# Kernel optimization log

Hardware: AMD Instinct MI355X
Metric: run time of the kernel (lower is better)

## Reference

```python
import jax, jax.numpy as jnp
import numpy as np

N_SRC = 100000
N_DST = 100000
E = 500000
D = 128
L = 2


def _sage(x_src, x_dst, e_src, e_dst, W_self, W_neigh, b):
    # DGL SAGEConv('mean'): out = x_dst @ W_self^T + mean_neighbors(x_src) @ W_neigh^T + b
    n_dst = x_dst.shape[0]
    msg_sum = jax.ops.segment_sum(x_src[e_src], e_dst, num_segments=n_dst)  # [n_dst, D]
    deg = jax.ops.segment_sum(jnp.ones((e_dst.shape[0],), x_src.dtype), e_dst, num_segments=n_dst)
    h_neigh = msg_sum / jnp.maximum(deg, 1.0)[:, None]  # isolated nodes -> 0
    return x_dst @ W_self.T + h_neigh @ W_neigh.T + b


def setup_inputs() -> dict:
    key = jax.random.key(0)
    ks = jax.random.split(key, 10)
    s = 1.0 / np.sqrt(D)
    return {
        "x_src": jax.random.normal(ks[0], (N_SRC, D), jnp.float32),
        "x_dst": jax.random.normal(ks[1], (N_DST, D), jnp.float32),
        "e_src": jax.random.randint(ks[2], (E,), 0, N_SRC, jnp.int32),
        "e_dst": jax.random.randint(ks[3], (E,), 0, N_DST, jnp.int32),
        "W_ship_self": jax.random.normal(ks[4], (L, D, D), jnp.float32) * s,
        "W_ship_neigh": jax.random.normal(ks[5], (L, D, D), jnp.float32) * s,
        "b_ship": jnp.zeros((L, D), jnp.float32),
        "W_rev_self": jax.random.normal(ks[6], (L, D, D), jnp.float32) * s,
        "W_rev_neigh": jax.random.normal(ks[7], (L, D, D), jnp.float32) * s,
        "b_rev": jnp.zeros((L, D), jnp.float32),
    }


def reference(x_src, x_dst, e_src, e_dst, W_ship_self, W_ship_neigh, b_ship,
              W_rev_self, W_rev_neigh, b_rev):
    h_s, h_d = x_src, x_dst
    n_layers = W_ship_self.shape[0]
    for l in range(n_layers):
        # ('source','ship','destination'): messages source -> destination
        new_d = _sage(h_s, h_d, e_src, e_dst, W_ship_self[l], W_ship_neigh[l], b_ship[l])
        # ('destination','rev_ship','source'): messages destination -> source
        new_s = _sage(h_d, h_s, e_dst, e_src, W_rev_self[l], W_rev_neigh[l], b_rev[l])
        h_d = jax.nn.relu(new_d)
        h_s = jax.nn.relu(new_s)
        # dropout p=0.0 (eval) -> identity
    return h_s, h_d
```

## Files before the change

kernel.cpp:

```cpp
#include <hip/hip_runtime.h>
#include <hip/hip_bf16.h>

#define NN 100000
#define EDGES 500000
#define DD 128
#define NBKT 196
#define SLACK 3584
#define CHUNK 4096
#define BPD ((EDGES + CHUNK - 1) / CHUNK)


typedef short bf16x8 __attribute__((ext_vector_type(8)));
typedef float f32x4  __attribute__((ext_vector_type(4)));
typedef float f32x2  __attribute__((ext_vector_type(2)));

__device__ __forceinline__ unsigned short f2bf(float f) {
    unsigned u = __float_as_uint(f);
    u += 0x7fffu + ((u >> 16) & 1u);
    return (unsigned short)(u >> 16);
}

__global__ void f2bx_kernel(const float* __restrict__ a, const float* __restrict__ b,
                            unsigned short* __restrict__ oaR, unsigned short* __restrict__ oaB,
                            unsigned short* __restrict__ obR, unsigned short* __restrict__ obB) {
    const float* in = blockIdx.y ? b : a;
    unsigned short* outR = blockIdx.y ? obR : oaR;
    unsigned short* outB = blockIdx.y ? obB : oaB;
    int t = blockIdx.x * 256 + threadIdx.x;
    int row = t >> 4, sl = t & 15;
    const float4* src = (const float4*)in + row * 32 + sl * 2;
    float4 v0 = src[0], v1 = src[1];
    uint4 o;
    o.x = (unsigned)f2bf(v0.x) | ((unsigned)f2bf(v0.y) << 16);
    o.y = (unsigned)f2bf(v0.z) | ((unsigned)f2bf(v0.w) << 16);
    o.z = (unsigned)f2bf(v1.x) | ((unsigned)f2bf(v1.y) << 16);
    o.w = (unsigned)f2bf(v1.z) | ((unsigned)f2bf(v1.w) << 16);
    *(uint4*)(outR + row * 128 + sl * 8) = o;
    int boff = (row >> 4) * 2048 + (sl >> 2) * 512 + (sl & 3) * 128 + (row & 15) * 8;
    *(uint4*)(outB + boff) = o;
}

__global__ void f2bw_kernel(const float* __restrict__ w0, const float* __restrict__ w1,
                            const float* __restrict__ w2, const float* __restrict__ w3,
                            unsigned short* __restrict__ o0, unsigned short* __restrict__ o1,
                            unsigned short* __restrict__ o2, unsigned short* __restrict__ o3) {
    const float* in; unsigned short* out;
    switch (blockIdx.y) {
        case 0: in = w0; out = o0; break;
        case 1: in = w1; out = o1; break;
        case 2: in = w2; out = o2; break;
        default: in = w3; out = o3; break;
    }
    int i = blockIdx.x * 256 + threadIdx.x;
    float4 v = ((const float4*)in)[i];
    ushort4 o;
    o.x = f2bf(v.x); o.y = f2bf(v.y); o.z = f2bf(v.z); o.w = f2bf(v.w);
    ((ushort4*)out)[i] = o;
}

__global__ __launch_bounds__(256) void bin_scatter_kernel(
    const int* __restrict__ e_src, const int* __restrict__ e_dst,
    int* __restrict__ gcnt,
    unsigned* __restrict__ recbin)
{
    const int dir = blockIdx.y;
    const int t = threadIdx.x;
    const int c0 = blockIdx.x * CHUNK;
    const int nvalid = min(CHUNK, EDGES - c0);
    const int* __restrict__ TGT = dir ? e_src : e_dst;
    const int* __restrict__ PAY = dir ? e_dst : e_src;

    __shared__ int hist[256];
    __shared__ int lbase[256];
    __shared__ int lofs[256];
    __shared__ int scanA[256], scanB[256];
    __shared__ int laddr[CHUNK];
    __shared__ unsigned lrec[CHUNK];

    hist[t] = 0;
    __syncthreads();

    int myb[16], myslot[16];
    unsigned myrec[16];
    #pragma unroll
    for (int j = 0; j < 16; ++j) {
        int e = c0 + j * 256 + t;
        myb[j] = -1;
        if (e < EDGES) {
            int tgt = TGT[e], pay = PAY[e];
            int b = tgt >> 9;
            myb[j] = b;
            myrec[j] = ((unsigned)pay << 9) | (unsigned)(tgt & 511);
            myslot[j] = atomicAdd(&hist[b], 1);
        }
    }
    __syncthreads();
    int cnt = hist[t];
    lbase[t] = (cnt > 0) ? atomicAdd(&gcnt[dir * 256 + t], cnt) : 0;
    scanA[t] = cnt;
    __syncthreads();
    int* pa = scanA; int* pb = scanB;
    for (int d = 1; d < 256; d <<= 1) {
        pb[t] = pa[t] + (t >= d ? pa[t - d] : 0);
        __syncthreads();
        int* tmp = pa; pa = pb; pb = tmp;
    }
    lofs[t] = pa[t] - cnt;
    __syncthreads();
    #pragma unroll
    for (int j = 0; j < 16; ++j) {
        if (myb[j] >= 0) {
            int b = myb[j];
            int pos = lofs[b] + myslot[j];
            int g = lbase[b] + myslot[j];
            lrec[pos] = myrec[j];
            laddr[pos] = (g < SLACK) ? (b * SLACK + g) : -1;
        }
    }
    __syncthreads();
    unsigned* __restrict__ out = recbin + (size_t)dir * NBKT * SLACK;
    #pragma unroll
    for (int j = 0; j < 16; ++j) {
        int i = j * 256 + t;
        if (i < nvalid) {
            int a = laddr[i];
            if (a >= 0) out[a] = lrec[i];
        }
    }
}

__global__ void bucket_scan_kernel(const int* __restrict__ gcnt, int* __restrict__ csr_base) {
    int t = threadIdx.x;
    __shared__ int A[256], B[256];
    for (int dir = 0; dir < 2; ++dir) {
        int c = (t < NBKT) ? min(gcnt[dir * 256 + t], SLACK) : 0;
        A[t] = c;
        __syncthreads();
        int* pa = A; int* pb = B;
        for (int d = 1; d < 256; d <<= 1) {
            pb[t] = pa[t] + (t >= d ? pa[t - d] : 0);
            __syncthreads();
            int* tmp = pa; pa = pb; pb = tmp;
        }
        if (t < NBKT) csr_base[dir * 200 + t] = pa[t] - c;
        if (t == 0)   csr_base[dir * 200 + NBKT] = pa[255];
        __syncthreads();
    }
}

__global__ __launch_bounds__(256) void fine_place_kernel(
    const unsigned* __restrict__ recbin, const int* __restrict__ gcnt,
    const int* __restrict__ csr_base,
    int* __restrict__ rp_dst, int* __restrict__ rp_src,
    float* __restrict__ inv_dst, float* __restrict__ inv_src,
    int* __restrict__ csr_dst, int* __restrict__ csr_src)
{
    const int dir = blockIdx.y;
    const int bkt = blockIdx.x;
    const int t = threadIdx.x;
    int*   __restrict__ rp  = dir ? rp_src  : rp_dst;
    float* __restrict__ inv = dir ? inv_src : inv_dst;
    int*   __restrict__ csr = dir ? csr_src : csr_dst;
    const unsigned* __restrict__ recs = recbin + ((size_t)dir * NBKT + bkt) * SLACK;
    const int cnt = min(gcnt[dir * 256 + bkt], SLACK);
    const int cbase = csr_base[dir * 200 + bkt];
    const int n0 = bkt * 512;

    __shared__ int deg[512];
    __shared__ int sA[512], sB[512];
    __shared__ int cur[512];
    deg[t] = 0; deg[t + 256] = 0;
    __syncthreads();
    for (int i = t; i < cnt; i += 256)
        atomicAdd(&deg[recs[i] & 511u], 1);
    __syncthreads();
    sA[t] = deg[t]; sA[t + 256] = deg[t + 256];
    __syncthreads();
    int* pa = sA; int* pb = sB;
    for (int d = 1; d < 512; d <<= 1) {
        pb[t]       = pa[t]       + (t >= d           ? pa[t - d]       : 0);
        pb[t + 256] = pa[t + 256] + ((t + 256) >= d   ? pa[t + 256 - d] : 0);
        __syncthreads();
        int* tmp = pa; pa = pb; pb = tmp;
    }
    #pragma unroll
    for (int k = 0; k < 2; ++k) {
        int i = t + k * 256;
        int off = pa[i] - deg[i];
        cur[i] = off;
        int node = n0 + i;
        if (node < NN) {
            rp[node] = cbase + off;
            inv[node] = 1.0f / (float)max(deg[i], 1);
        }
    }
    if (bkt == NBKT - 1 && t == 0) rp[NN] = csr_base[dir * 200 + NBKT];
    __syncthreads();
    for (int i = t; i < cnt; i += 256) {
        unsigned r = recs[i];
        int p = atomicAdd(&cur[r & 511u], 1);
        csr[cbase + p] = (int)(r >> 9);
    }
}

__global__ __launch_bounds__(256) void aggregate5_kernel(
    const unsigned short* __restrict__ h0, const int* __restrict__ rp0,
    const int* __restrict__ csr0, unsigned short* __restrict__ ag0,
    const unsigned short* __restrict__ h1, const int* __restrict__ rp1,
    const int* __restrict__ csr1, unsigned short* __restrict__ ag1)
{
    const int dir = blockIdx.y;
    const unsigned short* __restrict__ h = dir ? h1 : h0;
    const int* __restrict__ rp   = dir ? rp1 : rp0;
    const int* __restrict__ csr  = dir ? csr1 : csr0;
    unsigned short* __restrict__ agg = dir ? ag1 : ag0;

    const int t  = blockIdx.x * 256 + threadIdx.x;
    const int g  = t >> 4;
    const int sl = t & 15;

    const int beg = rp[g], end = rp[g + 1];
    const unsigned short* __restrict__ hp = h + sl * 8;

    f32x2 acc[4];
    #pragma unroll
    for (int k = 0; k < 4; ++k) acc[k] = (f32x2){0.f, 0.f};

    int cidx[8];
    #pragma unroll
    for (int j = 0; j < 8; ++j)
        cidx[j] = (beg + j < end) ? csr[beg + j] : -1;

    bf16x8 v[8];
    #pragma unroll
    for (int j = 0; j < 8; ++j)
        if (cidx[j] >= 0)
            v[j] = *(const bf16x8*)(hp + (size_t)cidx[j] * DD);

    #pragma unroll
    for (int j = 0; j < 8; ++j) {
        if (cidx[j] >= 0) {
            const unsigned* pu = (const unsigned*)&v[j];
            #pragma unroll
            for (int k = 0; k < 4; ++k) {
                unsigned u = pu[k];
                acc[k] += (f32x2){__uint_as_float(u << 16),
                                  __uint_as_float(u & 0xffff0000u)};
            }
        }
    }

    for (int i = beg + 8; i < end; ++i) {
        int c = csr[i];
        bf16x8 wv = *(const bf16x8*)(hp + (size_t)c * DD);
        const unsigned* pu = (const unsigned*)&wv;
        #pragma unroll
        for (int k = 0; k < 4; ++k) {
            unsigned u = pu[k];
            acc[k] += (f32x2){__uint_as_float(u << 16),
                              __uint_as_float(u & 0xffff0000u)};
        }
    }

    const float sc = 1.0f / (float)max(end - beg, 1);
    uint4 ov;
    ov.x = (unsigned)f2bf(acc[0].x * sc) | ((unsigned)f2bf(acc[0].y * sc) << 16);
    ov.y = (unsigned)f2bf(acc[1].x * sc) | ((unsigned)f2bf(acc[1].y * sc) << 16);
    ov.z = (unsigned)f2bf(acc[2].x * sc) | ((unsigned)f2bf(acc[2].y * sc) << 16);
    ov.w = (unsigned)f2bf(acc[3].x * sc) | ((unsigned)f2bf(acc[3].y * sc) << 16);
    int boff = (g >> 4) * 2048 + (sl >> 2) * 512 + (sl & 3) * 128 + (g & 15) * 8;
    *(uint4*)(agg + boff) = ov;
}

__global__ __launch_bounds__(512, 4) void mfma_gemm9_kernel(
    const unsigned short* __restrict__ Hs0, const unsigned short* __restrict__ Ha0,
    const unsigned short* __restrict__ Ws0, const unsigned short* __restrict__ Wn0,
    const float* __restrict__ bias0, float* __restrict__ outF0,
    unsigned short* __restrict__ outR0, unsigned short* __restrict__ outB0,
    const unsigned short* __restrict__ Hs1, const unsigned short* __restrict__ Ha1,
    const unsigned short* __restrict__ Ws1, const unsigned short* __restrict__ Wn1,
    const float* __restrict__ bias1, float* __restrict__ outF1,
    unsigned short* __restrict__ outR1, unsigned short* __restrict__ outB1,
    int M)
{
    const int dir = blockIdx.y;
    const unsigned short* __restrict__ Hself = dir ? Hs1 : Hs0;
    const unsigned short* __restrict__ Hagg  = dir ? Ha1 : Ha0;
    const unsigned short* __restrict__ Wself = dir ? Ws1 : Ws0;
    const unsigned short* __restrict__ Wneigh= dir ? Wn1 : Wn0;
    const float* __restrict__ bias = dir ? bias1 : bias0;
    float* __restrict__ outF = dir ? outF1 : outF0;
    unsigned short* __restrict__ outR = dir ? outR1 : outR0;
    unsigned short* __restrict__ outB = dir ? outB1 : outB0;

    __shared__ __align__(16) unsigned short sW[128 * 256];
    const int tid  = threadIdx.x;
    const int lane = tid & 63;
    const int w    = tid >> 6;
    const int row0 = blockIdx.x * 256;

    #pragma unroll
    for (int i = 0; i < 8; ++i) {
        int q = i * 512 + tid;
        int n = q >> 5, c = q & 31;
        const unsigned short* src = (c < 16) ? (Wself + n * 128 + c * 8)
                                             : (Wneigh + n * 128 + (c - 16) * 8);
        int d = n * 256 + (c & 24) * 8 + (((c ^ n) & 7) * 8);
        *(uint4*)(sW + d) = *(const uint4*)src;
    }

    const int mbase = (w >> 1) * 64;
    const int nbase = (w & 1) * 64;
    const int l15 = lane & 15;
    const int l4  = lane >> 4;
    const int MT  = M >> 4;

    int aoff[4];
    #pragma unroll
    for (int mt = 0; mt < 4; ++mt) {
        int rt = ((row0 + mbase) >> 4) + mt;
        if (rt >= MT) rt = MT - 1;
        aoff[mt] = rt * 2048 + lane * 8;
    }

    f32x4 acc[4][4];
    #pragma unroll
    for (int mt = 0; mt < 4; ++mt)
        #pragma unroll
        for (int nt = 0; nt < 4; ++nt) acc[mt][nt] = (f32x4){0.f, 0.f, 0.f, 0.f};

    __syncthreads();

    bf16x8 a_cur[4], a_nxt[4];
    #pragma unroll
    for (int mt = 0; mt < 4; ++mt) a_cur[mt] = *(const bf16x8*)(Hself + aoff[mt]);

    #pragma unroll
    for (int ks = 0; ks < 8; ++ks) {
        if (ks < 7) {
            const int ks1 = ks + 1;
            const int col = (ks1 & 3) * 512;
            const unsigned short* __restrict__ base = (ks1 < 4) ? Hself : Hagg;
            #pragma unroll
            for (int mt = 0; mt < 4; ++mt)
                a_nxt[mt] = *(const bf16x8*)(base + aoff[mt] + col);
        }
        const int c = ks * 4 + l4;
        bf16x8 b[4];
        #pragma unroll
        for (int nt = 0; nt < 4; ++nt) {
            int n = nbase + nt * 16 + l15;
            b[nt] = *(const bf16x8*)(sW + n * 256 + (c & 24) * 8 + (((c ^ n) & 7) * 8));
        }
        #pragma unroll
        for (int mt = 0; mt < 4; ++mt) {
            acc[mt][0] = __builtin_amdgcn_mfma_f32_16x16x32_bf16(a_cur[mt], b[0], acc[mt][0], 0, 0, 0);
            acc[mt][1] = __builtin_amdgcn_mfma_f32_16x16x32_bf16(a_cur[mt], b[1], acc[mt][1], 0, 0, 0);
            acc[mt][2] = __builtin_amdgcn_mfma_f32_16x16x32_bf16(a_cur[mt], b[2], acc[mt][2], 0, 0, 0);
            acc[mt][3] = __builtin_amdgcn_mfma_f32_16x16x32_bf16(a_cur[mt], b[3], acc[mt][3], 0, 0, 0);
        }
        #pragma unroll
        for (int mt = 0; mt < 4; ++mt) a_cur[mt] = a_nxt[mt];
    }

    #pragma unroll
    for (int nt = 0; nt < 4; ++nt) {
        int col = nbase + nt * 16 + l15;
        float bj = bias[col];
        #pragma unroll
        for (int mt = 0; mt < 4; ++mt) {
            #pragma unroll
            for (int r = 0; r < 4; ++r) {
                int grow = row0 + mbase + mt * 16 + l4 * 4 + r;
                if (grow < M) {
                    float v = fmaxf(acc[mt][nt][r] + bj, 0.f);
                    if (outF) {
                        outF[(size_t)grow * 128 + col] = v;
                    } else {
                        unsigned short bv = f2bf(v);
                        outR[(size_t)grow * 128 + col] = bv;
                        int bo = (grow >> 4) * 2048 + (col >> 5) * 512
                               + ((col >> 3) & 3) * 128 + (grow & 15) * 8 + (col & 7);
                        outB[bo] = bv;
                    }
                }
            }
        }
    }
}

extern "C" void kernel_launch(void* const* d_in, const int* in_sizes, int n_in,
                              void* d_out, int out_size, void* d_ws, size_t ws_size,
                              hipStream_t stream) {
    const float* x_src        = (const float*)d_in[0];
    const float* x_dst        = (const float*)d_in[1];
    const int*   e_src        = (const int*)d_in[2];
    const int*   e_dst        = (const int*)d_in[3];
    const float* W_ship_self  = (const float*)d_in[4];
    const float* W_ship_neigh = (const float*)d_in[5];
    const float* b_ship       = (const float*)d_in[6];
    const float* W_rev_self   = (const float*)d_in[7];
    const float* W_rev_neigh  = (const float*)d_in[8];
    const float* b_rev        = (const float*)d_in[9];
    float* out = (float*)d_out;

    char* ws = (char*)d_ws;
    size_t off = 0;
    auto alloc = [&](size_t bytes) {
        char* p = ws + off;
        off = (off + bytes + 255) & ~(size_t)255;
        return p;
    };
    unsigned short* xs_row = (unsigned short*)alloc((size_t)NN * DD * 2);
    unsigned short* xd_row = (unsigned short*)alloc((size_t)NN * DD * 2);
    unsigned short* xs_blk = (unsigned short*)alloc((size_t)NN * DD * 2);
    unsigned short* xd_blk = (unsigned short*)alloc((size_t)NN * DD * 2);
    unsigned short* agg1   = (unsigned short*)alloc((size_t)NN * DD * 2);
    unsigned short* agg2   = (unsigned short*)alloc((size_t)NN * DD * 2);
    unsigned short* Wss_bf = (unsigned short*)alloc(2 * DD * DD * 2);
    unsigned short* Wsn_bf = (unsigned short*)alloc(2 * DD * DD * 2);
    unsigned short* Wrs_bf = (unsigned short*)alloc(2 * DD * DD * 2);
    unsigned short* Wrn_bf = (unsigned short*)alloc(2 * DD * DD * 2);
    int* gcnt = (int*)alloc(2 * 256 * 4);
    int* csr_base = (int*)alloc(2 * 200 * 4);
    unsigned* recbin = (unsigned*)alloc((size_t)2 * NBKT * SLACK * 4);
    int* rp_dst = (int*)alloc((NN + 1) * 4);
    int* rp_src = (int*)alloc((NN + 1) * 4);
    float* inv_dst = (float*)alloc(NN * 4);
    float* inv_src = (float*)alloc(NN * 4);
    int* csr_dst = (int*)alloc(EDGES * 4);
    int* csr_src = (int*)alloc(EDGES * 4);
    (void)ws_size; (void)in_sizes; (void)n_in; (void)out_size;

    hipMemsetAsync(gcnt, 0, 2 * 256 * 4, stream);

    f2bx_kernel<<<dim3(NN * 16 / 256, 2), 256, 0, stream>>>(
        x_src, x_dst, xs_row, xs_blk, xd_row, xd_blk);
    f2bw_kernel<<<dim3(32, 4), 256, 0, stream>>>(W_ship_self, W_ship_neigh, W_rev_self, W_rev_neigh,
                                                 Wss_bf, Wsn_bf, Wrs_bf, Wrn_bf);

    bin_scatter_kernel<<<dim3(BPD, 2), 256, 0, stream>>>(e_src, e_dst, gcnt, recbin);
    bucket_scan_kernel<<<1, 256, 0, stream>>>(gcnt, csr_base);
    fine_place_kernel<<<dim3(NBKT, 2), 256, 0, stream>>>(recbin, gcnt, csr_base,
        rp_dst, rp_src, inv_dst, inv_src, csr_dst, csr_src);

    float* out_s = out;
    float* out_d = out + (size_t)NN * DD;
    const int gemm_grid = (NN + 255) / 256;
    const int agg_grid  = NN * 16 / 256;

    for (int l = 0; l < 2; ++l) {
        aggregate5_kernel<<<dim3(agg_grid, 2), 256, 0, stream>>>(
            xs_row, rp_dst, csr_dst, agg1,
            xd_row, rp_src, csr_src, agg2);
        mfma_gemm9_kernel<<<dim3(gemm_grid, 2), 512, 0, stream>>>(
            xd_blk, agg1, Wss_bf + l * DD * DD, Wsn_bf + l * DD * DD, b_ship + l * DD,
            l ? out_d : nullptr, xd_row, xd_blk,
            xs_blk, agg2, Wrs_bf + l * DD * DD, Wrn_bf + l * DD * DD, b_rev + l * DD,
            l ? out_s : nullptr, xs_row, xs_blk,
            NN);
    }
}
```

Baseline: 420.0 us.

## Fuse preprocessing kernels and convert weights to bf16 inside the GEMM

Merges the x bf16 conversion and the edge bin-scatter into one launch, and folds the bucket scan into fine_place by having each block redo the small 196-entry scan. Weight conversion moves into the GEMM prologue, which reads fp32 weights directly, and the A-tile prefetch is issued before that prologue. The unused inv_deg arrays are dropped and CHUNK is halved. The goal is fewer kernel launches and less serial launch overhead, at the cost of redundant scan and weight-conversion work in every block.

```diff
diff --git a/kernel.cpp b/kernel.cpp
--- a/kernel.cpp
+++ b/kernel.cpp
@@ -6,8 +6,9 @@
 #define DD 128
 #define NBKT 196
 #define SLACK 3584
-#define CHUNK 4096
+#define CHUNK 2048
 #define BPD ((EDGES + CHUNK - 1) / CHUNK)
+#define XBLK (NN * 16 / 256)
 
 
 typedef short bf16x8 __attribute__((ext_vector_type(8)));
@@ -20,55 +21,16 @@
     return (unsigned short)(u >> 16);
 }
 
-__global__ void f2bx_kernel(const float* __restrict__ a, const float* __restrict__ b,
-                            unsigned short* __restrict__ oaR, unsigned short* __restrict__ oaB,
-                            unsigned short* __restrict__ obR, unsigned short* __restrict__ obB) {
-    const float* in = blockIdx.y ? b : a;
-    unsigned short* outR = blockIdx.y ? obR : oaR;
-    unsigned short* outB = blockIdx.y ? obB : oaB;
-    int t = blockIdx.x * 256 + threadIdx.x;
-    int row = t >> 4, sl = t & 15;
-    const float4* src = (const float4*)in + row * 32 + sl * 2;
-    float4 v0 = src[0], v1 = src[1];
-    uint4 o;
-    o.x = (unsigned)f2bf(v0.x) | ((unsigned)f2bf(v0.y) << 16);
-    o.y = (unsigned)f2bf(v0.z) | ((unsigned)f2bf(v0.w) << 16);
-    o.z = (unsigned)f2bf(v1.x) | ((unsigned)f2bf(v1.y) << 16);
-    o.w = (unsigned)f2bf(v1.z) | ((unsigned)f2bf(v1.w) << 16);
-    *(uint4*)(outR + row * 128 + sl * 8) = o;
-    int boff = (row >> 4) * 2048 + (sl >> 2) * 512 + (sl & 3) * 128 + (row & 15) * 8;
-    *(uint4*)(outB + boff) = o;
-}
-
-__global__ void f2bw_kernel(const float* __restrict__ w0, const float* __restrict__ w1,
-                            const float* __restrict__ w2, const float* __restrict__ w3,
-                            unsigned short* __restrict__ o0, unsigned short* __restrict__ o1,
-                            unsigned short* __restrict__ o2, unsigned short* __restrict__ o3) {
-    const float* in; unsigned short* out;
-    switch (blockIdx.y) {
-        case 0: in = w0; out = o0; break;
-        case 1: in = w1; out = o1; break;
-        case 2: in = w2; out = o2; break;
-        default: in = w3; out = o3; break;
-    }
-    int i = blockIdx.x * 256 + threadIdx.x;
-    float4 v = ((const float4*)in)[i];
-    ushort4 o;
-    o.x = f2bf(v.x); o.y = f2bf(v.y); o.z = f2bf(v.z); o.w = f2bf(v.w);
-    ((ushort4*)out)[i] = o;
-}
-
-__global__ __launch_bounds__(256) void bin_scatter_kernel(
+__global__ __launch_bounds__(256) void prep_kernel(
+    const float* __restrict__ x_src, const float* __restrict__ x_dst,
+    unsigned short* __restrict__ xsR, unsigned short* __restrict__ xsB,
+    unsigned short* __restrict__ xdR, unsigned short* __restrict__ xdB,
     const int* __restrict__ e_src, const int* __restrict__ e_dst,
     int* __restrict__ gcnt,
     unsigned* __restrict__ recbin)
 {
-    const int dir = blockIdx.y;
+    const int bid = blockIdx.x;
     const int t = threadIdx.x;
-    const int c0 = blockIdx.x * CHUNK;
-    const int nvalid = min(CHUNK, EDGES - c0);
-    const int* __restrict__ TGT = dir ? e_src : e_dst;
-    const int* __restrict__ PAY = dir ? e_dst : e_src;
 
     __shared__ int hist[256];
     __shared__ int lbase[256];
@@ -77,98 +39,115 @@
     __shared__ int laddr[CHUNK];
     __shared__ unsigned lrec[CHUNK];
 
-    hist[t] = 0;
-    __syncthreads();
-
-    int myb[16], myslot[16];
-    unsigned myrec[16];
-    #pragma unroll
-    for (int j = 0; j < 16; ++j) {
-        int e = c0 + j * 256 + t;
-        myb[j] = -1;
-        if (e < EDGES) {
-            int tgt = TGT[e], pay = PAY[e];
-            int b = tgt >> 9;
-            myb[j] = b;
-            myrec[j] = ((unsigned)pay << 9) | (unsigned)(tgt & 511);
-            myslot[j] = atomicAdd(&hist[b], 1);
-        }
-    }
-    __syncthreads();
-    int cnt = hist[t];
-    lbase[t] = (cnt > 0) ? atomicAdd(&gcnt[dir * 256 + t], cnt) : 0;
-    scanA[t] = cnt;
-    __syncthreads();
-    int* pa = scanA; int* pb = scanB;
-    for (int d = 1; d < 256; d <<= 1) {
-        pb[t] = pa[t] + (t >= d ? pa[t - d] : 0);
-        __syncthreads();
-        int* tmp = pa; pa = pb; pb = tmp;
-    }
-    lofs[t] = pa[t] - cnt;
-    __syncthreads();
-    #pragma unroll
-    for (int j = 0; j < 16; ++j) {
-        if (myb[j] >= 0) {
-            int b = myb[j];
-            int pos = lofs[b] + myslot[j];
-            int g = lbase[b] + myslot[j];
-            lrec[pos] = myrec[j];
-            laddr[pos] = (g < SLACK) ? (b * SLACK + g) : -1;
-        }
-    }
-    __syncthreads();
-    unsigned* __restrict__ out = recbin + (size_t)dir * NBKT * SLACK;
-    #pragma unroll
-    for (int j = 0; j < 16; ++j) {
-        int i = j * 256 + t;
-        if (i < nvalid) {
-            int a = laddr[i];
-            if (a >= 0) out[a] = lrec[i];
-        }
-    }
-}
-
-__global__ void bucket_scan_kernel(const int* __restrict__ gcnt, int* __restrict__ csr_base) {
-    int t = threadIdx.x;
-    __shared__ int A[256], B[256];
-    for (int dir = 0; dir < 2; ++dir) {
-        int c = (t < NBKT) ? min(gcnt[dir * 256 + t], SLACK) : 0;
-        A[t] = c;
-        __syncthreads();
-        int* pa = A; int* pb = B;
+    if (bid < 2 * BPD) {
+        const int dir = (bid >= BPD) ? 1 : 0;
+        const int c0 = (dir ? bid - BPD : bid) * CHUNK;
+        const int nvalid = min(CHUNK, EDGES - c0);
+        const int* __restrict__ TGT = dir ? e_src : e_dst;
+        const int* __restrict__ PAY = dir ? e_dst : e_src;
+
+        hist[t] = 0;
+        __syncthreads();
+
+        int myb[8], myslot[8];
+        unsigned myrec[8];
+        #pragma unroll
+        for (int j = 0; j < 8; ++j) {
+            int e = c0 + j * 256 + t;
+            myb[j] = -1;
+            if (e < EDGES) {
+                int tgt = TGT[e], pay = PAY[e];
+                int b = tgt >> 9;
+                myb[j] = b;
+                myrec[j] = ((unsigned)pay << 9) | (unsigned)(tgt & 511);
+                myslot[j] = atomicAdd(&hist[b], 1);
+            }
+        }
+        __syncthreads();
+        int cnt = hist[t];
+        lbase[t] = (cnt > 0) ? atomicAdd(&gcnt[dir * 256 + t], cnt) : 0;
+        scanA[t] = cnt;
+        __syncthreads();
+        int* pa = scanA; int* pb = scanB;
         for (int d = 1; d < 256; d <<= 1) {
             pb[t] = pa[t] + (t >= d ? pa[t - d] : 0);
             __syncthreads();
             int* tmp = pa; pa = pb; pb = tmp;
         }
-        if (t < NBKT) csr_base[dir * 200 + t] = pa[t] - c;
-        if (t == 0)   csr_base[dir * 200 + NBKT] = pa[255];
-        __syncthreads();
-    }
-}
-
-__global__ __launch_bounds__(256) void fine_place_kernel(
+        lofs[t] = pa[t] - cnt;
+        __syncthreads();
+        #pragma unroll
+        for (int j = 0; j < 8; ++j) {
+            if (myb[j] >= 0) {
+                int b = myb[j];
+                int pos = lofs[b] + myslot[j];
+                int g = lbase[b] + myslot[j];
+                lrec[pos] = myrec[j];
+                laddr[pos] = (g < SLACK) ? (b * SLACK + g) : -1;
+            }
+        }
+        __syncthreads();
+        unsigned* __restrict__ out = recbin + (size_t)dir * NBKT * SLACK;
+        #pragma unroll
+        for (int j = 0; j < 8; ++j) {
+            int i = j * 256 + t;
+            if (i < nvalid) {
+                int a = laddr[i];
+                if (a >= 0) out[a] = lrec[i];
+            }
+        }
+    } else {
+        int q = bid - 2 * BPD;
+        const float* in; unsigned short* outR; unsigned short* outB;
+        if (q < XBLK) { in = x_src; outR = xsR; outB = xsB; }
+        else          { in = x_dst; outR = xdR; outB = xdB; q -= XBLK; }
+        int tt = q * 256 + t;
+        int row = tt >> 4, sl = tt & 15;
+        const float4* src = (const float4*)in + row * 32 + sl * 2;
+        float4 v0 = src[0], v1 = src[1];
+        uint4 o;
+        o.x = (unsigned)f2bf(v0.x) | ((unsigned)f2bf(v0.y) << 16);
+        o.y = (unsigned)f2bf(v0.z) | ((unsigned)f2bf(v0.w) << 16);
+        o.z = (unsigned)f2bf(v1.x) | ((unsigned)f2bf(v1.y) << 16);
+        o.w = (unsigned)f2bf(v1.z) | ((unsigned)f2bf(v1.w) << 16);
+        *(uint4*)(outR + row * 128 + sl * 8) = o;
+        int boff = (row >> 4) * 2048 + (sl >> 2) * 512 + (sl & 3) * 128 + (row & 15) * 8;
+        *(uint4*)(outB + boff) = o;
+    }
+}
+
+__global__ __launch_bounds__(256) void fine_place2_kernel(
     const unsigned* __restrict__ recbin, const int* __restrict__ gcnt,
-    const int* __restrict__ csr_base,
     int* __restrict__ rp_dst, int* __restrict__ rp_src,
-    float* __restrict__ inv_dst, float* __restrict__ inv_src,
     int* __restrict__ csr_dst, int* __restrict__ csr_src)
 {
     const int dir = blockIdx.y;
     const int bkt = blockIdx.x;
     const int t = threadIdx.x;
-    int*   __restrict__ rp  = dir ? rp_src  : rp_dst;
-    float* __restrict__ inv = dir ? inv_src : inv_dst;
-    int*   __restrict__ csr = dir ? csr_src : csr_dst;
+    int* __restrict__ rp  = dir ? rp_src  : rp_dst;
+    int* __restrict__ csr = dir ? csr_src : csr_dst;
     const unsigned* __restrict__ recs = recbin + ((size_t)dir * NBKT + bkt) * SLACK;
     const int cnt = min(gcnt[dir * 256 + bkt], SLACK);
-    const int cbase = csr_base[dir * 200 + bkt];
     const int n0 = bkt * 512;
 
     __shared__ int deg[512];
     __shared__ int sA[512], sB[512];
     __shared__ int cur[512];
+
+    sA[t] = (t < NBKT) ? min(gcnt[dir * 256 + t], SLACK) : 0;
+    __syncthreads();
+    {
+        int* pa = sA; int* pb = sB;
+        for (int d = 1; d < 256; d <<= 1) {
+            pb[t] = pa[t] + (t >= d ? pa[t - d] : 0);
+            __syncthreads();
+            int* tmp = pa; pa = pb; pb = tmp;
+        }
+    }
+    const int cbase = sA[bkt] - cnt;
+    const int total = sA[255];
+    __syncthreads();
+
     deg[t] = 0; deg[t + 256] = 0;
     __syncthreads();
     for (int i = t; i < cnt; i += 256)
@@ -189,12 +168,9 @@
         int off = pa[i] - deg[i];
         cur[i] = off;
         int node = n0 + i;
-        if (node < NN) {
-            rp[node] = cbase + off;
-            inv[node] = 1.0f / (float)max(deg[i], 1);
-        }
-    }
-    if (bkt == NBKT - 1 && t == 0) rp[NN] = csr_base[dir * 200 + NBKT];
+        if (node < NN) rp[node] = cbase + off;
+    }
+    if (bkt == NBKT - 1 && t == 0) rp[NN] = total;
     __syncthreads();
     for (int i = t; i < cnt; i += 256) {
         unsigned r = recs[i];
@@ -272,13 +248,13 @@
     *(uint4*)(agg + boff) = ov;
 }
 
-__global__ __launch_bounds__(512, 4) void mfma_gemm9_kernel(
+__global__ __launch_bounds__(512, 4) void mfma_gemm10_kernel(
     const unsigned short* __restrict__ Hs0, const unsigned short* __restrict__ Ha0,
-    const unsigned short* __restrict__ Ws0, const unsigned short* __restrict__ Wn0,
+    const float* __restrict__ Ws0, const float* __restrict__ Wn0,
     const float* __restrict__ bias0, float* __restrict__ outF0,
     unsigned short* __restrict__ outR0, unsigned short* __restrict__ outB0,
     const unsigned short* __restrict__ Hs1, const unsigned short* __restrict__ Ha1,
-    const unsigned short* __restrict__ Ws1, const unsigned short* __restrict__ Wn1,
+    const float* __restrict__ Ws1, const float* __restrict__ Wn1,
     const float* __restrict__ bias1, float* __restrict__ outF1,
     unsigned short* __restrict__ outR1, unsigned short* __restrict__ outB1,
     int M)
@@ -286,8 +262,8 @@
     const int dir = blockIdx.y;
     const unsigned short* __restrict__ Hself = dir ? Hs1 : Hs0;
     const unsigned short* __restrict__ Hagg  = dir ? Ha1 : Ha0;
-    const unsigned short* __restrict__ Wself = dir ? Ws1 : Ws0;
-    const unsigned short* __restrict__ Wneigh= dir ? Wn1 : Wn0;
+    const float* __restrict__ Wself = dir ? Ws1 : Ws0;
+    const float* __restrict__ Wneigh= dir ? Wn1 : Wn0;
     const float* __restrict__ bias = dir ? bias1 : bias0;
     float* __restrict__ outF = dir ? outF1 : outF0;
     unsigned short* __restrict__ outR = dir ? outR1 : outR0;
@@ -299,16 +275,6 @@
     const int w    = tid >> 6;
     const int row0 = blockIdx.x * 256;
 
-    #pragma unroll
-    for (int i = 0; i < 8; ++i) {
-        int q = i * 512 + tid;
-        int n = q >> 5, c = q & 31;
-        const unsigned short* src = (c < 16) ? (Wself + n * 128 + c * 8)
-                                             : (Wneigh + n * 128 + (c - 16) * 8);
-        int d = n * 256 + (c & 24) * 8 + (((c ^ n) & 7) * 8);
-        *(uint4*)(sW + d) = *(const uint4*)src;
-    }
-
     const int mbase = (w >> 1) * 64;
     const int nbase = (w & 1) * 64;
     const int l15 = lane & 15;
@@ -323,6 +289,27 @@
         aoff[mt] = rt * 2048 + lane * 8;
     }
 
+    bf16x8 a_cur[4], a_nxt[4];
+    #pragma unroll
+    for (int mt = 0; mt < 4; ++mt) a_cur[mt] = *(const bf16x8*)(Hself + aoff[mt]);
+
+    #pragma unroll
+    for (int i = 0; i < 8; ++i) {
+        int q = i * 512 + tid;
+        int n = q >> 5, c = q & 31;
+        const float* src = (c < 16) ? (Wself  + n * 128 + (c & 15) * 8)
+                                    : (Wneigh + n * 128 + (c - 16) * 8);
+        float4 v0 = *(const float4*)src;
+        float4 v1 = *(const float4*)(src + 4);
+        uint4 o;
+        o.x = (unsigned)f2bf(v0.x) | ((unsigned)f2bf(v0.y) << 16);
+        o.y = (unsigned)f2bf(v0.z) | ((unsigned)f2bf(v0.w) << 16);
+        o.z = (unsigned)f2bf(v1.x) | ((unsigned)f2bf(v1.y) << 16);
+        o.w = (unsigned)f2bf(v1.z) | ((unsigned)f2bf(v1.w) << 16);
+        int d = n * 256 + (c & 24) * 8 + (((c ^ n) & 7) * 8);
+        *(uint4*)(sW + d) = o;
+    }
+
     f32x4 acc[4][4];
     #pragma unroll
     for (int mt = 0; mt < 4; ++mt)
@@ -330,10 +317,6 @@
         for (int nt = 0; nt < 4; ++nt) acc[mt][nt] = (f32x4){0.f, 0.f, 0.f, 0.f};
 
     __syncthreads();
-
-    bf16x8 a_cur[4], a_nxt[4];
-    #pragma unroll
-    for (int mt = 0; mt < 4; ++mt) a_cur[mt] = *(const bf16x8*)(Hself + aoff[mt]);
 
     #pragma unroll
     for (int ks = 0; ks < 8; ++ks) {
@@ -417,32 +400,22 @@
     unsigned short* xd_blk = (unsigned short*)alloc((size_t)NN * DD * 2);
     unsigned short* agg1   = (unsigned short*)alloc((size_t)NN * DD * 2);
     unsigned short* agg2   = (unsigned short*)alloc((size_t)NN * DD * 2);
-    unsigned short* Wss_bf = (unsigned short*)alloc(2 * DD * DD * 2);
-    unsigned short* Wsn_bf = (unsigned short*)alloc(2 * DD * DD * 2);
-    unsigned short* Wrs_bf = (unsigned short*)alloc(2 * DD * DD * 2);
-    unsigned short* Wrn_bf = (unsigned short*)alloc(2 * DD * DD * 2);
     int* gcnt = (int*)alloc(2 * 256 * 4);
-    int* csr_base = (int*)alloc(2 * 200 * 4);
     unsigned* recbin = (unsigned*)alloc((size_t)2 * NBKT * SLACK * 4);
     int* rp_dst = (int*)alloc((NN + 1) * 4);
     int* rp_src = (int*)alloc((NN + 1) * 4);
-    float* inv_dst = (float*)alloc(NN * 4);
-    float* inv_src = (float*)alloc(NN * 4);
     int* csr_dst = (int*)alloc(EDGES * 4);
     int* csr_src = (int*)alloc(EDGES * 4);
     (void)ws_size; (void)in_sizes; (void)n_in; (void)out_size;
 
     hipMemsetAsync(gcnt, 0, 2 * 256 * 4, stream);
 
-    f2bx_kernel<<<dim3(NN * 16 / 256, 2), 256, 0, stream>>>(
-        x_src, x_dst, xs_row, xs_blk, xd_row, xd_blk);
-    f2bw_kernel<<<dim3(32, 4), 256, 0, stream>>>(W_ship_self, W_ship_neigh, W_rev_self, W_rev_neigh,
-                                                 Wss_bf, Wsn_bf, Wrs_bf, Wrn_bf);
-
-    bin_scatter_kernel<<<dim3(BPD, 2), 256, 0, stream>>>(e_src, e_dst, gcnt, recbin);
-    bucket_scan_kernel<<<1, 256, 0, stream>>>(gcnt, csr_base);
-    fine_place_kernel<<<dim3(NBKT, 2), 256, 0, stream>>>(recbin, gcnt, csr_base,
-        rp_dst, rp_src, inv_dst, inv_src, csr_dst, csr_src);
+    prep_kernel<<<2 * BPD + 2 * XBLK, 256, 0, stream>>>(
+        x_src, x_dst, xs_row, xs_blk, xd_row, xd_blk,
+        e_src, e_dst, gcnt, recbin);
+
+    fine_place2_kernel<<<dim3(NBKT, 2), 256, 0, stream>>>(
+        recbin, gcnt, rp_dst, rp_src, csr_dst, csr_src);
 
     float* out_s = out;
     float* out_d = out + (size_t)NN * DD;
@@ -453,10 +426,10 @@
         aggregate5_kernel<<<dim3(agg_grid, 2), 256, 0, stream>>>(
             xs_row, rp_dst, csr_dst, agg1,
             xd_row, rp_src, csr_src, agg2);
-        mfma_gemm9_kernel<<<dim3(gemm_grid, 2), 512, 0, stream>>>(
-            xd_blk, agg1, Wss_bf + l * DD * DD, Wsn_bf + l * DD * DD, b_ship + l * DD,
+        mfma_gemm10_kernel<<<dim3(gemm_grid, 2), 512, 0, stream>>>(
+            xd_blk, agg1, W_ship_self + l * DD * DD, W_ship_neigh + l * DD * DD, b_ship + l * DD,
             l ? out_d : nullptr, xd_row, xd_blk,
-            xs_blk, agg2, Wrs_bf + l * DD * DD, Wrn_bf + l * DD * DD, b_rev + l * DD,
+            xs_blk, agg2, W_rev_self + l * DD * DD, W_rev_neigh + l * DD * DD, b_rev + l * DD,
             l ? out_s : nullptr, xs_row, xs_blk,
             NN);
     }
```

Result: faster. 410.4 us (-2.3%).
